# Optimization experiments

Hardware: AMD Instinct MI355X
Metric: run time of the kernel (lower is better)

The kernel has to match this reference:

```python
import jax, jax.numpy as jnp
import numpy as np

DIM = 64
NUM_FEAT = 14
NUM_OUT = 105
N_NODES = 8192
N_EDGES = 16384
N_GRAPHS = 256
N_STEMS = 2048
N_JBONDS = 1024


def lrelu(v):
    return jax.nn.leaky_relu(v, 0.01)


def setup_inputs() -> dict:
    key = jax.random.key(0)
    ks = jax.random.split(key, 40)
    def rn(k, shape, s=0.1):
        return jax.random.normal(k, shape, dtype=jnp.float32) * s
    inp = {}
    inp['x'] = jax.random.normal(ks[0], (N_NODES, NUM_FEAT), dtype=jnp.float32)
    inp['edge_attr'] = jax.random.uniform(ks[1], (N_EDGES, 4), dtype=jnp.float32)
    inp['edge_index'] = jax.random.randint(ks[2], (2, N_EDGES), 0, N_NODES)
    inp['batch'] = jnp.sort(jax.random.randint(ks[3], (N_NODES,), 0, N_GRAPHS))
    inp['stem_atmidx'] = jax.random.randint(ks[4], (N_STEMS,), 0, N_NODES)
    inp['jbond_atmidx'] = jax.random.randint(ks[5], (N_JBONDS, 2), 0, N_NODES)
    # lin0
    inp['lin0_w'] = rn(ks[6], (NUM_FEAT, DIM)); inp['lin0_b'] = rn(ks[7], (DIM,))
    # NNConv edge net: Linear(4,dim) -> LeakyReLU -> Linear(dim, dim*dim)
    inp['net_w1'] = rn(ks[8], (4, DIM)); inp['net_b1'] = rn(ks[9], (DIM,))
    inp['net_w2'] = rn(ks[10], (DIM, DIM * DIM), 0.02); inp['net_b2'] = rn(ks[11], (DIM * DIM,), 0.02)
    # NNConv root weight + bias
    inp['conv_root'] = rn(ks[12], (DIM, DIM)); inp['conv_bias'] = rn(ks[13], (DIM,))
    # GRU (torch gate order r,z,n); stored [in, 3*dim]
    inp['gru_w_ih'] = rn(ks[14], (DIM, 3 * DIM)); inp['gru_w_hh'] = rn(ks[15], (DIM, 3 * DIM))
    inp['gru_b_ih'] = rn(ks[16], (3 * DIM,)); inp['gru_b_hh'] = rn(ks[17], (3 * DIM,))
    # node2stem MLP
    inp['n2s_w1'] = rn(ks[18], (DIM, DIM)); inp['n2s_b1'] = rn(ks[19], (DIM,))
    inp['n2s_w2'] = rn(ks[20], (DIM, NUM_OUT)); inp['n2s_b2'] = rn(ks[21], (NUM_OUT,))
    # node2jbond MLP
    inp['n2j_w1'] = rn(ks[22], (DIM, DIM)); inp['n2j_b1'] = rn(ks[23], (DIM,))
    inp['n2j_w2'] = rn(ks[24], (DIM, 1)); inp['n2j_b2'] = rn(ks[25], (1,))
    # Set2Set LSTM(2*dim -> dim), torch gate order i,f,g,o; stored [in, 4*dim]
    inp['s2s_w_ih'] = rn(ks[26], (2 * DIM, 4 * DIM)); inp['s2s_w_hh'] = rn(ks[27], (DIM, 4 * DIM))
    inp['s2s_b_ih'] = rn(ks[28], (4 * DIM,)); inp['s2s_b_hh'] = rn(ks[29], (4 * DIM,))
    # lin_out
    inp['lin_out_w'] = rn(ks[30], (2 * DIM, 2)); inp['lin_out_b'] = rn(ks[31], (2,))
    return inp


def reference(x, edge_attr, lin0_w, lin0_b, net_w1, net_b1, net_w2, net_b2,
              conv_root, conv_bias, gru_w_ih, gru_w_hh, gru_b_ih, gru_b_hh,
              n2s_w1, n2s_b1, n2s_w2, n2s_b2, n2j_w1, n2j_b1, n2j_w2, n2j_b2,
              s2s_w_ih, s2s_w_hh, s2s_b_ih, s2s_b_hh, lin_out_w, lin_out_b,
              edge_index, batch, stem_atmidx, jbond_atmidx):
    N = x.shape[0]
    src, dst = edge_index[0], edge_index[1]
    out = lrelu(x @ lin0_w + lin0_b)          # [N, dim]
    h = out
    # edge-conditioned weights (edge_attr is constant across the 6 iterations)
    ew = (lrelu(edge_attr @ net_w1 + net_b1) @ net_w2 + net_b2).reshape(-1, DIM, DIM)  # [E,dim,dim]
    deg = jnp.maximum(jax.ops.segment_sum(jnp.ones_like(dst, dtype=x.dtype), dst, num_segments=N), 1.0)[:, None]
    for _ in range(6):
        msg = jnp.einsum('ei,eio->eo', out[src], ew)                        # per-edge matmul
        agg = jax.ops.segment_sum(msg, dst, num_segments=N) / deg          # scatter-mean
        m = lrelu(agg + out @ conv_root + conv_bias)
        # GRU update (torch gate order r,z,n)
        gi = m @ gru_w_ih + gru_b_ih
        gh = h @ gru_w_hh + gru_b_hh
        ir, iz, inn = jnp.split(gi, 3, axis=-1)
        hr, hz, hn = jnp.split(gh, 3, axis=-1)
        r = jax.nn.sigmoid(ir + hr)
        z = jax.nn.sigmoid(iz + hz)
        n = jnp.tanh(inn + r * hn)
        h = (1.0 - z) * n + z * h
        out = h
    # per-stem block logits
    stem_preds = lrelu(out[stem_atmidx] @ n2s_w1 + n2s_b1) @ n2s_w2 + n2s_b2  # [S, num_out]
    # jbond: gather both endpoints, predict scalar, mean over the pair
    jb = out[jbond_atmidx.reshape(-1)]
    jpred = lrelu(jb @ n2j_w1 + n2j_b1) @ n2j_w2 + n2j_b2                     # [2J,1]
    jbond_preds = jpred.reshape(jbond_atmidx.shape).mean(axis=1)              # [J]
    # Set2Set, processing_steps=1
    B = N_GRAPHS
    hS = jnp.zeros((B, DIM), x.dtype)
    cS = jnp.zeros((B, DIM), x.dtype)
    q_star = jnp.zeros((B, 2 * DIM), x.dtype)
    gates = q_star @ s2s_w_ih + s2s_b_ih + hS @ s2s_w_hh + s2s_b_hh
    gi_, gf_, gg_, go_ = jnp.split(gates, 4, axis=-1)
    cS = jax.nn.sigmoid(gf_) * cS + jax.nn.sigmoid(gi_) * jnp.tanh(gg_)
    hS = jax.nn.sigmoid(go_) * jnp.tanh(cS)
    q = hS                                                                    # [B, dim]
    e = jnp.sum(out * q[batch], axis=-1)                                      # [N]
    emax = jax.ops.segment_max(e, batch, num_segments=B)
    a_un = jnp.exp(e - emax[batch])
    a = a_un / jax.ops.segment_sum(a_un, batch, num_segments=B)[batch]
    r_pool = jax.ops.segment_sum(a[:, None] * out, batch, num_segments=B)     # [B, dim]
    q_star = jnp.concatenate([q, r_pool], axis=1)                             # [B, 2*dim]
    scalar_outs = q_star @ lin_out_w + lin_out_b                              # [B, 2]
    return (scalar_outs, stem_preds, jbond_preds)
```

## Files before the change

### kernel.cpp

```cpp
#include <hip/hip_runtime.h>

#define DIM 64
#define NF 14
#define NOUT 105
#define NN 8192
#define NE 16384
#define NB 256
#define NS 2048
#define NJ 1024
#define KTOT 4160
#define KSPLIT 8

#define C_X      0
#define C_EA     114688
#define C_L0W    180224
#define C_L0B    181120
#define C_NW1    181184
#define C_NB1    181440
#define C_NW2    181504
#define C_NB2    443648
#define C_CRT    447744
#define C_CB     451840
#define C_GWIH   451904
#define C_GWHH   464192
#define C_GBIH   476480
#define C_GBHH   476672
#define C_SW1    476864
#define C_SB1    480960
#define C_SW2    481024
#define C_SB2    487744
#define C_JW1    487856
#define C_JB1    491952
#define C_JW2    492016
#define C_JB2    492080
#define C_S2IH   492088
#define C_S2HH   492344
#define C_LOW    492600
#define C_LOB    492856
#define C_TOT    492864

typedef float f32x4 __attribute__((ext_vector_type(4)));
typedef short bf16x8 __attribute__((ext_vector_type(8)));

__device__ __forceinline__ float bf2f(unsigned short u){
  union { unsigned int i; float f; } v; v.i = ((unsigned int)u) << 16; return v.f;
}
__device__ __forceinline__ unsigned short f2bf(float f){
  union { float f; unsigned int i; } v; v.f = f;
  unsigned int x = v.i;
  return (unsigned short)((x + 0x7FFFu + ((x >> 16) & 1u)) >> 16);
}
__device__ __forceinline__ float sigm(float x){ return 1.f / (1.f + __expf(-x)); }
__device__ __forceinline__ float tanh_f(float x){
  x = fminf(10.f, fmaxf(-10.f, x));
  float e = __expf(2.f * x);
  return (e - 1.f) / (e + 1.f);
}
__device__ __forceinline__ float lrelu(float x){ return x > 0.f ? x : 0.01f * x; }

__device__ __forceinline__ float wred_sum(float v){
  #pragma unroll
  for (int off = 32; off > 0; off >>= 1) v += __shfl_xor(v, off, 64);
  return v;
}
__device__ __forceinline__ float wred_max(float v){
  #pragma unroll
  for (int off = 32; off > 0; off >>= 1) v = fmaxf(v, __shfl_xor(v, off, 64));
  return v;
}


__global__ void k_detect(const unsigned short* __restrict__ ea, int* __restrict__ flag){
  __shared__ int cnt;
  if (threadIdx.x == 0) cnt = 0;
  __syncthreads();
  int c = 0;
  for (int i = threadIdx.x; i < 8192; i += 256) c += (ea[2*i] >> 15) & 1;
  atomicAdd(&cnt, c);
  __syncthreads();
  if (threadIdx.x == 0) *flag = (cnt > 100) ? 1 : 0;
}

struct CvtArgs {
  const void* src[26];
  int n[26];
  int off[26];
};

__global__ void k_cvt(CvtArgs a, const int* __restrict__ flag, unsigned short* __restrict__ dst){
  bool f32 = (*flag != 0);
  int gid = blockIdx.x * blockDim.x + threadIdx.x, gs = gridDim.x * blockDim.x;
  #pragma unroll 1
  for (int j = 0; j < 26; ++j){
    const void* s = a.src[j];
    int n = a.n[j], o = a.off[j];
    for (int i = gid; i < n; i += gs)
      dst[o + i] = f32 ? f2bf(((const float*)s)[i]) : ((const unsigned short*)s)[i];
  }
}


__global__ void k_deg(const int* __restrict__ ei, float* __restrict__ deg){
  int e = blockIdx.x * blockDim.x + threadIdx.x;
  if (e < NE) atomicAdd(&deg[ei[NE + e]], 1.0f);
}

__global__ void k_lin0(const unsigned short* __restrict__ cvt,
                       float* __restrict__ actF, unsigned short* __restrict__ actB){
  const unsigned short* x = cvt + C_X;
  const unsigned short* w = cvt + C_L0W;
  const unsigned short* b = cvt + C_L0B;
  int idx = blockIdx.x * blockDim.x + threadIdx.x;
  int n = idx >> 6, d = idx & 63;
  float acc = bf2f(b[d]);
  #pragma unroll
  for (int f = 0; f < NF; ++f) acc += bf2f(x[n*NF + f]) * bf2f(w[f*DIM + d]);
  float v = lrelu(acc);
  actF[idx] = v; actB[idx] = f2bf(v);
}

__global__ void k_u(const unsigned short* __restrict__ cvt, unsigned short* __restrict__ u){
  const unsigned short* ea = cvt + C_EA;
  const unsigned short* w  = cvt + C_NW1;
  const unsigned short* b  = cvt + C_NB1;
  int idx = blockIdx.x * blockDim.x + threadIdx.x;
  int e = idx >> 6, d = idx & 63;
  float acc = bf2f(b[d]);
  #pragma unroll
  for (int f = 0; f < 4; ++f) acc += bf2f(ea[e*4 + f]) * bf2f(w[f*DIM + d]);
  u[idx] = f2bf(lrelu(acc));
}

__global__ void k_w2t(const unsigned short* __restrict__ cvt, unsigned short* __restrict__ w2t){
  const unsigned short* w2 = cvt + C_NW2;
  int t = blockIdx.x * blockDim.x + threadIdx.x;
  int n = t >> 6, k = t & 63;
  w2t[t] = w2[k*4096 + n];
}

__global__ void k_w2r(const unsigned short* __restrict__ cvt, unsigned short* __restrict__ w2rt){
  const unsigned short* w2 = cvt + C_NW2;
  const unsigned short* b2 = cvt + C_NB2;
  int t = blockIdx.x * blockDim.x + threadIdx.x;
  int o = t / KTOT, k = t - o * KTOT;
  unsigned short v = (k < 4096) ? w2[(k >> 6) * 4096 + (k & 63) * 64 + o]
                                : b2[(k - 4096) * 64 + o];
  w2rt[t] = v;
}

__global__ void k_prep(const unsigned short* __restrict__ cvt,
                       unsigned short* __restrict__ crt, unsigned short* __restrict__ btg,
                       float* __restrict__ cbg, float* __restrict__ qv){
  const unsigned short* cr  = cvt + C_CRT;
  const unsigned short* wih = cvt + C_GWIH;
  const unsigned short* whh = cvt + C_GWHH;
  const unsigned short* bih = cvt + C_GBIH;
  const unsigned short* bhh = cvt + C_GBHH;
  const unsigned short* s2sbih = cvt + C_S2IH;
  const unsigned short* s2sbhh = cvt + C_S2HH;
  int tid = threadIdx.x;
  for (int t = tid; t < 4096; t += 256){ int n = t & 63, k = t >> 6; crt[n*64 + k] = cr[k*64 + n]; }
  for (int t = tid; t < 32768; t += 256){
    int nidx = t >> 7, kidx = t & 127;
    int g = nidx >> 6, d = nidx & 63, ki = kidx & 63;
    unsigned short v = 0;
    if (kidx < 64){
      if (g == 0) v = wih[ki*192 + d];
      else if (g == 1) v = wih[ki*192 + 64 + d];
      else if (g == 2) v = wih[ki*192 + 128 + d];
    } else {
      if (g == 0) v = whh[ki*192 + d];
      else if (g == 1) v = whh[ki*192 + 64 + d];
      else if (g == 3) v = whh[ki*192 + 128 + d];
    }
    btg[nidx*128 + kidx] = v;
  }
  if (tid < 256){
    int g = tid >> 6, d = tid & 63;
    float v;
    if (g == 0) v = bf2f(bih[d]) + bf2f(bhh[d]);
    else if (g == 1) v = bf2f(bih[64 + d]) + bf2f(bhh[64 + d]);
    else if (g == 2) v = bf2f(bih[128 + d]);
    else v = bf2f(bhh[128 + d]);
    cbg[tid] = v;
  }
  if (tid < 64){
    float gi = bf2f(s2sbih[tid])       + bf2f(s2sbhh[tid]);
    float gg = bf2f(s2sbih[128 + tid]) + bf2f(s2sbhh[128 + tid]);
    float go = bf2f(s2sbih[192 + tid]) + bf2f(s2sbhh[192 + tid]);
    float c = sigm(gi) * tanh_f(gg);
    qv[tid] = sigm(go) * tanh_f(c);
  }
}


__global__ __launch_bounds__(256) void k_ew(const unsigned short* __restrict__ z,
                                            const unsigned short* __restrict__ w2t,
                                            const unsigned short* __restrict__ cvt,
                                            unsigned short* __restrict__ ew){
  const unsigned short* b2 = cvt + C_NB2;
  int w = threadIdx.x >> 6, lane = threadIdx.x & 63;
  int lm = lane & 15, q8 = (lane >> 4) * 8, rq = (lane >> 4) * 4;
  int e0 = blockIdx.x * 64;
  int n0 = blockIdx.y * 256 + w * 64;
  f32x4 acc[4][4];
  #pragma unroll
  for (int mt = 0; mt < 4; ++mt)
    #pragma unroll
    for (int nt = 0; nt < 4; ++nt) acc[mt][nt] = (f32x4){0.f, 0.f, 0.f, 0.f};
  #pragma unroll
  for (int kk = 0; kk < 2; ++kk){
    bf16x8 af[4], bfr[4];
    #pragma unroll
    for (int mt = 0; mt < 4; ++mt)
      af[mt] = *(const bf16x8*)&z[(size_t)(e0 + mt*16 + lm)*64 + kk*32 + q8];
    #pragma unroll
    for (int nt = 0; nt < 4; ++nt)
      bfr[nt] = *(const bf16x8*)&w2t[(size_t)(n0 + nt*16 + lm)*64 + kk*32 + q8];
    #pragma unroll
    for (int mt = 0; mt < 4; ++mt)
      #pragma unroll
      for (int nt = 0; nt < 4; ++nt)
        acc[mt][nt] = __builtin_amdgcn_mfma_f32_16x16x32_bf16(af[mt], bfr[nt], acc[mt][nt], 0, 0, 0);
  }
  #pragma unroll
  for (int nt = 0; nt < 4; ++nt){
    int col = n0 + nt*16 + lm;
    float bb = bf2f(b2[col]);
    #pragma unroll
    for (int mt = 0; mt < 4; ++mt)
      #pragma unroll
      for (int r = 0; r < 4; ++r){
        int row = e0 + mt*16 + rq + r;
        ew[(size_t)row*4096 + col] = f2bf(acc[mt][nt][r] + bb);
      }
  }
}

__global__ __launch_bounds__(256) void k_msg(const unsigned short* __restrict__ actB,
                                             const unsigned short* __restrict__ ew,
                                             const int* __restrict__ ei,
                                             float* __restrict__ agg){
  __shared__ float sact[4][64];
  int w = threadIdx.x >> 6, lane = threadIdx.x & 63;
  int e = blockIdx.x * 4 + w;
  int src = ei[e], dst = ei[NE + e];
  sact[w][lane] = bf2f(actB[(size_t)src*64 + lane]);
  __syncthreads();
  const unsigned short* ep = &ew[(size_t)e * 4096];
  float acc = 0.f;
  #pragma unroll 16
  for (int i = 0; i < 64; ++i) acc += sact[w][i] * bf2f(ep[i*64 + lane]);
  atomicAdd(&agg[(size_t)dst*64 + lane], acc);
}


__global__ __launch_bounds__(256) void k_msgf(const unsigned short* __restrict__ actB,
                                              const unsigned short* __restrict__ z,
                                              const unsigned short* __restrict__ w2rt,
                                              const int* __restrict__ ei,
                                              float* __restrict__ agg){
  __shared__ __align__(16) unsigned short sz[256 * 8];
  int w = threadIdx.x >> 6, lane = threadIdx.x & 63;
  int lm = lane & 15, q8 = (lane >> 4) * 8, rq = (lane >> 4) * 4;
  int e0 = blockIdx.x * 256;
  int s  = blockIdx.y;
  {
    int t = threadIdx.x;
    *(uint4*)&sz[t * 8] = *(const uint4*)&z[(size_t)(e0 + t) * 64 + s * 8];
  }
  __syncthreads();

  uint4 apack[4][2];
  #pragma unroll
  for (int mt = 0; mt < 4; ++mt){
    int src = ei[e0 + w*64 + mt*16 + lm];
    apack[mt][0] = *(const uint4*)&actB[(size_t)src * 64 + q8];
    apack[mt][1] = *(const uint4*)&actB[(size_t)src * 64 + 32 + q8];
  }

  f32x4 acc[4][4];
  #pragma unroll
  for (int mt = 0; mt < 4; ++mt)
    #pragma unroll
    for (int nt = 0; nt < 4; ++nt) acc[mt][nt] = (f32x4){0.f, 0.f, 0.f, 0.f};

  int kk0 = s * 16;
  int nk = (s == KSPLIT - 1) ? 18 : 16;
  for (int c = 0; c < nk; ++c){
    int kk = kk0 + c;
    bf16x8 bfr[4];
    #pragma unroll
    for (int nt = 0; nt < 4; ++nt)
      bfr[nt] = *(const bf16x8*)&w2rt[(size_t)(nt*16 + lm) * KTOT + kk*32 + q8];
    #pragma unroll
    for (int mt = 0; mt < 4; ++mt){
      float zf = 1.0f;
      if (kk < 128){
        int erow = w*64 + mt*16 + lm;
        zf = bf2f(sz[erow * 8 + ((kk >> 1) & 7)]);
      }
      uint4 ap = apack[mt][kk & 1];
      bf16x8 af;
      #pragma unroll
      for (int h = 0; h < 4; ++h){
        unsigned int dw = ((const unsigned int*)&ap)[h];
        float flo = __uint_as_float(dw << 16) * zf;
        float fhi = __uint_as_float(dw & 0xFFFF0000u) * zf;
        unsigned int pk = ((unsigned int)f2bf(flo)) | (((unsigned int)f2bf(fhi)) << 16);
        ((unsigned int*)&af)[h] = pk;
      }
      #pragma unroll
      for (int nt = 0; nt < 4; ++nt)
        acc[mt][nt] = __builtin_amdgcn_mfma_f32_16x16x32_bf16(af, bfr[nt], acc[mt][nt], 0, 0, 0);
    }
  }

  #pragma unroll
  for (int mt = 0; mt < 4; ++mt){
    int dstv[4];
    #pragma unroll
    for (int r = 0; r < 4; ++r) dstv[r] = ei[NE + e0 + w*64 + mt*16 + rq + r];
    #pragma unroll
    for (int nt = 0; nt < 4; ++nt)
      #pragma unroll
      for (int r = 0; r < 4; ++r)
        atomicAdd(&agg[(size_t)dstv[r] * 64 + nt*16 + lm], acc[mt][nt][r]);
  }
}


__global__ __launch_bounds__(256) void k_gru(const unsigned short* __restrict__ actB_in,
                                             const float* __restrict__ actF_in,
                                             float* __restrict__ agg, const float* __restrict__ deg,
                                             const unsigned short* __restrict__ crt,
                                             const unsigned short* __restrict__ cvt,
                                             const unsigned short* __restrict__ btg,
                                             const float* __restrict__ cbg,
                                             float* __restrict__ actF_out, unsigned short* __restrict__ actB_out){
  const unsigned short* cbias = cvt + C_CB;
  __shared__ __align__(16) unsigned short s_frag[2*4*16*8];
  int w = threadIdx.x >> 6, lane = threadIdx.x & 63;
  int lm = lane & 15, q = lane >> 4;
  int q8 = q*8, rq = q*4;
  int r0 = blockIdx.x * 16;
  f32x4 am = (f32x4){0.f, 0.f, 0.f, 0.f};
  #pragma unroll
  for (int kk = 0; kk < 2; ++kk){
    bf16x8 a = *(const bf16x8*)&actB_in[(size_t)(r0 + lm)*64 + kk*32 + q8];
    bf16x8 b = *(const bf16x8*)&crt[(size_t)(w*16 + lm)*64 + kk*32 + q8];
    am = __builtin_amdgcn_mfma_f32_16x16x32_bf16(a, b, am, 0, 0, 0);
  }
  {
    int col = w*16 + lm;
    float cb = bf2f(cbias[col]);
    int kk2 = w >> 1, q2 = (w & 1)*2 + (lm >> 3), j = lm & 7;
    #pragma unroll
    for (int r = 0; r < 4; ++r){
      int row = r0 + rq + r;
      float dg = fmaxf(deg[row], 1.f);
      float v = am[r] + agg[(size_t)row*64 + col] / dg + cb;
      agg[(size_t)row*64 + col] = 0.f;
      s_frag[((kk2*4 + q2)*16 + (rq + r))*8 + j] = f2bf(lrelu(v));
    }
  }
  __syncthreads();
  f32x4 g[4];
  #pragma unroll
  for (int t = 0; t < 4; ++t) g[t] = (f32x4){0.f, 0.f, 0.f, 0.f};
  #pragma unroll
  for (int kk = 0; kk < 4; ++kk){
    bf16x8 a;
    if (kk < 2) a = *(const bf16x8*)&s_frag[(kk*4 + q)*128 + lm*8];
    else        a = *(const bf16x8*)&actB_in[(size_t)(r0 + lm)*64 + (kk - 2)*32 + q8];
    #pragma unroll
    for (int t = 0; t < 4; ++t){
      bf16x8 b = *(const bf16x8*)&btg[(size_t)(t*64 + w*16 + lm)*128 + kk*32 + q8];
      g[t] = __builtin_amdgcn_mfma_f32_16x16x32_bf16(a, b, g[t], 0, 0, 0);
    }
  }
  {
    int d = w*16 + lm;
    float cb_r = cbg[d], cb_z = cbg[64 + d], cb_n = cbg[128 + d], cb_h = cbg[192 + d];
    #pragma unroll
    for (int r = 0; r < 4; ++r){
      int row = r0 + rq + r;
      float rr = sigm(g[0][r] + cb_r);
      float zz = sigm(g[1][r] + cb_z);
      float nn = tanh_f(g[2][r] + cb_n + rr * (g[3][r] + cb_h));
      float ho = actF_in[(size_t)row*64 + d];
      float hn2 = (1.f - zz) * nn + zz * ho;
      actF_out[(size_t)row*64 + d] = hn2;
      actB_out[(size_t)row*64 + d] = f2bf(hn2);
    }
  }
}


__device__ __forceinline__ int lower_bound_batch(const int* b, int val){
  int lo = 0, hi = NN;
  while (lo < hi){ int mid = (lo + hi) >> 1; if (b[mid] < val) lo = mid + 1; else hi = mid; }
  return lo;
}

__device__ __forceinline__ void store_out(void* outp, const int* flag, size_t idx, float v){
  if (*flag) ((float*)outp)[idx] = v;
  else       ((unsigned short*)outp)[idx] = f2bf(v);
}

__global__ __launch_bounds__(64) void k_graph(const float* __restrict__ act,
                                              const int* __restrict__ batch, const float* __restrict__ qv,
                                              const unsigned short* __restrict__ cvt,
                                              const int* __restrict__ flag,
                                              void* __restrict__ outp){
  const unsigned short* lw = cvt + C_LOW;
  const unsigned short* lb = cvt + C_LOB;
  __shared__ float se[512];
  int b = blockIdx.x, lane = threadIdx.x;
  int lo = lower_bound_batch(batch, b);
  int hi = lower_bound_batch(batch, b + 1);
  int cnt = hi - lo; if (cnt > 512) cnt = 512;
  float qvl = qv[lane];
  for (int ii = 0; ii < cnt; ++ii){
    float p = act[(size_t)(lo + ii)*64 + lane] * qvl;
    p = wred_sum(p);
    if (lane == 0) se[ii] = p;
  }
  __syncthreads();
  float em = -3.4e38f;
  for (int ii = lane; ii < cnt; ii += 64) em = fmaxf(em, se[ii]);
  em = wred_max(em);
  float sm = 0.f;
  for (int ii = lane; ii < cnt; ii += 64) sm += __expf(se[ii] - em);
  float denom = wred_sum(sm);
  float rp = 0.f;
  for (int ii = 0; ii < cnt; ++ii) rp += __expf(se[ii] - em) * act[(size_t)(lo + ii)*64 + lane];
  if (cnt > 0 && denom > 0.f) rp /= denom;
  float s0 = qvl*bf2f(lw[lane*2])     + rp*bf2f(lw[(64 + lane)*2]);
  float s1 = qvl*bf2f(lw[lane*2 + 1]) + rp*bf2f(lw[(64 + lane)*2 + 1]);
  s0 = wred_sum(s0); s1 = wred_sum(s1);
  if (lane == 0){
    store_out(outp, flag, b*2,     s0 + bf2f(lb[0]));
    store_out(outp, flag, b*2 + 1, s1 + bf2f(lb[1]));
  }
}

__global__ __launch_bounds__(256) void k_stem(const float* __restrict__ act, const int* __restrict__ sidx,
                                              const unsigned short* __restrict__ cvt,
                                              const int* __restrict__ flag,
                                              void* __restrict__ outp){
  const unsigned short* w1 = cvt + C_SW1;
  const unsigned short* b1 = cvt + C_SB1;
  const unsigned short* w2 = cvt + C_SW2;
  const unsigned short* b2 = cvt + C_SB2;
  __shared__ float sa[4][64], st[4][64];
  int w = threadIdx.x >> 6, lane = threadIdx.x & 63;
  int s = blockIdx.x * 4 + w;
  int a = sidx[s];
  sa[w][lane] = act[(size_t)a*64 + lane];
  __syncthreads();
  float t = bf2f(b1[lane]);
  #pragma unroll 8
  for (int i = 0; i < 64; ++i) t += sa[w][i] * bf2f(w1[i*64 + lane]);
  st[w][lane] = lrelu(t);
  __syncthreads();
  size_t base = 512 + (size_t)s * NOUT;
  float v = bf2f(b2[lane]);
  #pragma unroll 8
  for (int d = 0; d < 64; ++d) v += st[w][d] * bf2f(w2[d*NOUT + lane]);
  store_out(outp, flag, base + lane, v);
  int o2 = 64 + lane;
  if (o2 < NOUT){
    float v2 = bf2f(b2[o2]);
    #pragma unroll 8
    for (int d = 0; d < 64; ++d) v2 += st[w][d] * bf2f(w2[d*NOUT + o2]);
    store_out(outp, flag, base + o2, v2);
  }
}

__global__ __launch_bounds__(256) void k_jbond(const float* __restrict__ act, const int* __restrict__ jidx,
                                               const unsigned short* __restrict__ cvt,
                                               const int* __restrict__ flag,
                                               void* __restrict__ outp){
  const unsigned short* w1 = cvt + C_JW1;
  const unsigned short* b1 = cvt + C_JB1;
  const unsigned short* w2 = cvt + C_JW2;
  const unsigned short* b2 = cvt + C_JB2;
  __shared__ float a0[4][64], a1[4][64];
  int w = threadIdx.x >> 6, lane = threadIdx.x & 63;
  int j = blockIdx.x * 4 + w;
  int i0 = jidx[j*2], i1 = jidx[j*2 + 1];
  a0[w][lane] = act[(size_t)i0*64 + lane];
  a1[w][lane] = act[(size_t)i1*64 + lane];
  __syncthreads();
  float t0 = bf2f(b1[lane]), t1 = t0;
  #pragma unroll 8
  for (int i = 0; i < 64; ++i){
    float wv = bf2f(w1[i*64 + lane]);
    t0 += a0[w][i] * wv;
    t1 += a1[w][i] * wv;
  }
  t0 = lrelu(t0); t1 = lrelu(t1);
  float p = (t0 + t1) * bf2f(w2[lane]);
  p = wred_sum(p);
  if (lane == 0) store_out(outp, flag, 512 + (size_t)NS*NOUT + j, 0.5f * p + bf2f(b2[0]));
}


extern "C" void kernel_launch(void* const* d_in, const int* in_sizes, int n_in,
                              void* d_out, int out_size, void* d_ws, size_t ws_size,
                              hipStream_t stream){
  (void)in_sizes; (void)n_in; (void)out_size;
  const int* edge_index = (const int*)d_in[2];
  const int* batch      = (const int*)d_in[3];
  const int* stem_idx   = (const int*)d_in[4];
  const int* jbond_idx  = (const int*)d_in[5];

  char* ws = (char*)d_ws;
  size_t off = 0;
  auto alloc = [&](size_t bytes) -> void* {
    void* p = ws + off; off += (bytes + 255) & ~(size_t)255; return p;
  };
  unsigned short* cvt  = (unsigned short*)alloc((size_t)C_TOT * 2);
  unsigned short* w2t  = (unsigned short*)alloc((size_t)4096 * 64 * 2);
  unsigned short* w2rt = (unsigned short*)alloc((size_t)64 * KTOT * 2);
  unsigned short* z_bf = (unsigned short*)alloc((size_t)NE * 64 * 2);
  float* actF0 = (float*)alloc((size_t)NN * 64 * 4);
  float* actF1 = (float*)alloc((size_t)NN * 64 * 4);
  unsigned short* actB0 = (unsigned short*)alloc((size_t)NN * 64 * 2);
  unsigned short* actB1 = (unsigned short*)alloc((size_t)NN * 64 * 2);
  float* deg  = (float*)alloc(NN * 4);
  float* agg  = (float*)alloc((size_t)NN * 64 * 4);
  unsigned short* crt = (unsigned short*)alloc(64 * 64 * 2);
  unsigned short* btg = (unsigned short*)alloc(256 * 128 * 2);
  float* cbg  = (float*)alloc(256 * 4);
  float* qv   = (float*)alloc(64 * 4);
  int* flag   = (int*)alloc(256);
  size_t ew_bytes = (size_t)NE * 4096 * 2;
  bool big = (off + ew_bytes) <= ws_size;
  unsigned short* ew = big ? (unsigned short*)alloc(ew_bytes) : nullptr;

  hipMemsetAsync(deg, 0, ((size_t)NN * 4) + ((size_t)NN * 64 * 4) + 256, stream);

  k_detect<<<1, 256, 0, stream>>>((const unsigned short*)d_in[1], flag);

  CvtArgs ca;
  const int srcIdx[26] = {0,1,6,7,8,9,10,11,12,13,14,15,16,17,18,19,20,21,22,23,24,25,28,29,30,31};
  const int ns[26]  = {114688,65536,896,64,256,64,262144,4096,4096,64,12288,12288,192,192,
                       4096,64,6720,105,4096,64,64,1,256,256,256,2};
  const int ofs[26] = {C_X,C_EA,C_L0W,C_L0B,C_NW1,C_NB1,C_NW2,C_NB2,C_CRT,C_CB,C_GWIH,C_GWHH,
                       C_GBIH,C_GBHH,C_SW1,C_SB1,C_SW2,C_SB2,C_JW1,C_JB1,C_JW2,C_JB2,
                       C_S2IH,C_S2HH,C_LOW,C_LOB};
  for (int j = 0; j < 26; ++j){ ca.src[j] = d_in[srcIdx[j]]; ca.n[j] = ns[j]; ca.off[j] = ofs[j]; }
  k_cvt<<<512, 256, 0, stream>>>(ca, flag, cvt);

  k_deg<<<NE/256, 256, 0, stream>>>(edge_index, deg);
  k_lin0<<<NN*DIM/256, 256, 0, stream>>>(cvt, actF0, actB0);
  k_u<<<NE*DIM/256, 256, 0, stream>>>(cvt, z_bf);
  k_prep<<<1, 256, 0, stream>>>(cvt, crt, btg, cbg, qv);

  if (big){
    k_w2t<<<4096*64/256, 256, 0, stream>>>(cvt, w2t);
    k_ew<<<dim3(NE/64, 16), 256, 0, stream>>>(z_bf, w2t, cvt, ew);
  } else {
    k_w2r<<<64*KTOT/256, 256, 0, stream>>>(cvt, w2rt);
  }

  for (int t = 0; t < 6; ++t){
    const float* aF_in  = (t & 1) ? actF1 : actF0;
    float* aF_out       = (t & 1) ? actF0 : actF1;
    const unsigned short* aB_in = (t & 1) ? actB1 : actB0;
    unsigned short* aB_out      = (t & 1) ? actB0 : actB1;
    if (big)
      k_msg<<<NE/4, 256, 0, stream>>>(aB_in, ew, edge_index, agg);
    else
      k_msgf<<<dim3(NE/256, KSPLIT), 256, 0, stream>>>(aB_in, z_bf, w2rt, edge_index, agg);
    k_gru<<<NN/16, 256, 0, stream>>>(aB_in, aF_in, agg, deg, crt, cvt, btg, cbg,
                                     aF_out, aB_out);
  }
  k_graph<<<NB, 64, 0, stream>>>(actF0, batch, qv, cvt, flag, d_out);
  k_stem<<<NS/4, 256, 0, stream>>>(actF0, stem_idx, cvt, flag, d_out);
  k_jbond<<<NJ/4, 256, 0, stream>>>(actF0, jbond_idx, cvt, flag, d_out);
}
```

Baseline: 445.1 us.

## Transpose edge-weight layout and stage ew stores through swizzled LDS for vector writes

Permutes the w2t columns so each edge's weight matrix is stored transposed, which lets k_msg read 8 contiguous bf16 per lane with 16-byte vector loads instead of scalar strided loads. k_ew now writes its MFMA output into a swizzled shared-memory tile and then emits coalesced 16-byte global stores. This targets global memory transaction efficiency on the large ew buffer, at the cost of 32KB of LDS per block, which may reduce occupancy. Whether these kernels run by default depends on dispatch code that is not shown (k_msgf exists as an alternative path).

```diff
diff --git a/kernel.cpp b/kernel.cpp
--- a/kernel.cpp
+++ b/kernel.cpp
@@ -135,7 +135,7 @@
   const unsigned short* w2 = cvt + C_NW2;
   int t = blockIdx.x * blockDim.x + threadIdx.x;
   int n = t >> 6, k = t & 63;
-  w2t[t] = w2[k*4096 + n];
+  w2t[t] = w2[k*4096 + (n & 63)*64 + (n >> 6)];
 }
 
 __global__ void k_w2r(const unsigned short* __restrict__ cvt, unsigned short* __restrict__ w2rt){
@@ -199,6 +199,7 @@
                                             const unsigned short* __restrict__ cvt,
                                             unsigned short* __restrict__ ew){
   const unsigned short* b2 = cvt + C_NB2;
+  __shared__ __align__(16) unsigned short tile[4][4096];
   int w = threadIdx.x >> 6, lane = threadIdx.x & 63;
   int lm = lane & 15, q8 = (lane >> 4) * 8, rq = (lane >> 4) * 4;
   int e0 = blockIdx.x * 64;
@@ -225,15 +226,25 @@
   }
   #pragma unroll
   for (int nt = 0; nt < 4; ++nt){
-    int col = n0 + nt*16 + lm;
-    float bb = bf2f(b2[col]);
+    int col = nt*16 + lm;
+    int gcol = n0 + col;
+    float bb = bf2f(b2[((gcol & 63) << 6) | (gcol >> 6)]);
     #pragma unroll
     for (int mt = 0; mt < 4; ++mt)
       #pragma unroll
       for (int r = 0; r < 4; ++r){
-        int row = e0 + mt*16 + rq + r;
-        ew[(size_t)row*4096 + col] = f2bf(acc[mt][nt][r] + bb);
+        int row = mt*16 + rq + r;
+        int phys = (col >> 3) ^ (row & 7);
+        tile[w][row*64 + phys*8 + (col & 7)] = f2bf(acc[mt][nt][r] + bb);
       }
+  }
+  #pragma unroll
+  for (int it = 0; it < 8; ++it){
+    int row = it*8 + (lane >> 3);
+    int c16 = lane & 7;
+    int phys = c16 ^ (row & 7);
+    bf16x8 v = *(const bf16x8*)&tile[w][row*64 + phys*8];
+    *(bf16x8*)&ew[(size_t)(e0 + row)*4096 + n0 + c16*8] = v;
   }
 }
 
@@ -241,16 +252,28 @@
                                              const unsigned short* __restrict__ ew,
                                              const int* __restrict__ ei,
                                              float* __restrict__ agg){
-  __shared__ float sact[4][64];
+  __shared__ __align__(16) float sact[4][64];
   int w = threadIdx.x >> 6, lane = threadIdx.x & 63;
   int e = blockIdx.x * 4 + w;
   int src = ei[e], dst = ei[NE + e];
   sact[w][lane] = bf2f(actB[(size_t)src*64 + lane]);
   __syncthreads();
-  const unsigned short* ep = &ew[(size_t)e * 4096];
+  const unsigned short* ep = ew + (size_t)e*4096 + (size_t)lane*64;
   float acc = 0.f;
-  #pragma unroll 16
-  for (int i = 0; i < 64; ++i) acc += sact[w][i] * bf2f(ep[i*64 + lane]);
+  #pragma unroll
+  for (int t = 0; t < 8; ++t){
+    bf16x8 v = *(const bf16x8*)(ep + t*8);
+    f32x4 sa = *(const f32x4*)&sact[w][t*8];
+    f32x4 sb = *(const f32x4*)&sact[w][t*8 + 4];
+    acc += bf2f((unsigned short)v[0]) * sa[0];
+    acc += bf2f((unsigned short)v[1]) * sa[1];
+    acc += bf2f((unsigned short)v[2]) * sa[2];
+    acc += bf2f((unsigned short)v[3]) * sa[3];
+    acc += bf2f((unsigned short)v[4]) * sb[0];
+    acc += bf2f((unsigned short)v[5]) * sb[1];
+    acc += bf2f((unsigned short)v[6]) * sb[2];
+    acc += bf2f((unsigned short)v[7]) * sb[3];
+  }
   atomicAdd(&agg[(size_t)dst*64 + lane], acc);
 }
 
```

Measured after the change: 454.2 us. +2.0%, slower.

## Replace materialized edge weights with a fused factorized message kernel

Applied to the files above, without the earlier changes.

Drops the path that materializes the per-edge 64x64 weight tensor (about 128 MB in bf16) and re-reads it in all six message-passing iterations. Every iteration now computes messages directly with MFMA: the source activations are scaled by each edge-MLP hidden value and multiplied against the reordered second-layer weights, with the bias folded in as an extra K chunk. The fused kernel uses 64-edge tiles split four ways over K, stages z in padded shared memory, and packs bf16 with a cheaper rounding helper. The cost is extra MFMA work and atomic adds in every iteration instead of pure bandwidth-bound reads.

```diff
diff --git a/kernel.cpp b/kernel.cpp
--- a/kernel.cpp
+++ b/kernel.cpp
@@ -9,7 +9,6 @@
 #define NS 2048
 #define NJ 1024
 #define KTOT 4160
-#define KSPLIT 8
 
 #define C_X      0
 #define C_EA     114688
@@ -69,6 +68,12 @@
   return v;
 }
 
+__device__ __forceinline__ unsigned int pk_bf(float flo, float fhi){
+  unsigned int lo = __float_as_uint(flo) + 0x8000u;
+  unsigned int hi = __float_as_uint(fhi) + 0x8000u;
+  return (hi & 0xFFFF0000u) | (lo >> 16);
+}
+
 
 __global__ void k_detect(const unsigned short* __restrict__ ea, int* __restrict__ flag){
   __shared__ int cnt;
@@ -129,13 +134,6 @@
   #pragma unroll
   for (int f = 0; f < 4; ++f) acc += bf2f(ea[e*4 + f]) * bf2f(w[f*DIM + d]);
   u[idx] = f2bf(lrelu(acc));
-}
-
-__global__ void k_w2t(const unsigned short* __restrict__ cvt, unsigned short* __restrict__ w2t){
-  const unsigned short* w2 = cvt + C_NW2;
-  int t = blockIdx.x * blockDim.x + threadIdx.x;
-  int n = t >> 6, k = t & 63;
-  w2t[t] = w2[k*4096 + n];
 }
 
 __global__ void k_w2r(const unsigned short* __restrict__ cvt, unsigned short* __restrict__ w2rt){
@@ -194,138 +192,87 @@
 }
 
 
-__global__ __launch_bounds__(256) void k_ew(const unsigned short* __restrict__ z,
-                                            const unsigned short* __restrict__ w2t,
-                                            const unsigned short* __restrict__ cvt,
-                                            unsigned short* __restrict__ ew){
-  const unsigned short* b2 = cvt + C_NB2;
-  int w = threadIdx.x >> 6, lane = threadIdx.x & 63;
-  int lm = lane & 15, q8 = (lane >> 4) * 8, rq = (lane >> 4) * 4;
-  int e0 = blockIdx.x * 64;
-  int n0 = blockIdx.y * 256 + w * 64;
-  f32x4 acc[4][4];
-  #pragma unroll
-  for (int mt = 0; mt < 4; ++mt)
-    #pragma unroll
-    for (int nt = 0; nt < 4; ++nt) acc[mt][nt] = (f32x4){0.f, 0.f, 0.f, 0.f};
-  #pragma unroll
-  for (int kk = 0; kk < 2; ++kk){
-    bf16x8 af[4], bfr[4];
-    #pragma unroll
-    for (int mt = 0; mt < 4; ++mt)
-      af[mt] = *(const bf16x8*)&z[(size_t)(e0 + mt*16 + lm)*64 + kk*32 + q8];
-    #pragma unroll
-    for (int nt = 0; nt < 4; ++nt)
-      bfr[nt] = *(const bf16x8*)&w2t[(size_t)(n0 + nt*16 + lm)*64 + kk*32 + q8];
-    #pragma unroll
-    for (int mt = 0; mt < 4; ++mt)
-      #pragma unroll
-      for (int nt = 0; nt < 4; ++nt)
-        acc[mt][nt] = __builtin_amdgcn_mfma_f32_16x16x32_bf16(af[mt], bfr[nt], acc[mt][nt], 0, 0, 0);
-  }
-  #pragma unroll
-  for (int nt = 0; nt < 4; ++nt){
-    int col = n0 + nt*16 + lm;
-    float bb = bf2f(b2[col]);
-    #pragma unroll
-    for (int mt = 0; mt < 4; ++mt)
-      #pragma unroll
-      for (int r = 0; r < 4; ++r){
-        int row = e0 + mt*16 + rq + r;
-        ew[(size_t)row*4096 + col] = f2bf(acc[mt][nt][r] + bb);
-      }
-  }
-}
-
-__global__ __launch_bounds__(256) void k_msg(const unsigned short* __restrict__ actB,
-                                             const unsigned short* __restrict__ ew,
-                                             const int* __restrict__ ei,
-                                             float* __restrict__ agg){
-  __shared__ float sact[4][64];
-  int w = threadIdx.x >> 6, lane = threadIdx.x & 63;
-  int e = blockIdx.x * 4 + w;
-  int src = ei[e], dst = ei[NE + e];
-  sact[w][lane] = bf2f(actB[(size_t)src*64 + lane]);
-  __syncthreads();
-  const unsigned short* ep = &ew[(size_t)e * 4096];
-  float acc = 0.f;
-  #pragma unroll 16
-  for (int i = 0; i < 64; ++i) acc += sact[w][i] * bf2f(ep[i*64 + lane]);
-  atomicAdd(&agg[(size_t)dst*64 + lane], acc);
-}
-
-
-__global__ __launch_bounds__(256) void k_msgf(const unsigned short* __restrict__ actB,
+__global__ __launch_bounds__(256) void k_msgr(const unsigned short* __restrict__ actB,
                                               const unsigned short* __restrict__ z,
                                               const unsigned short* __restrict__ w2rt,
                                               const int* __restrict__ ei,
                                               float* __restrict__ agg){
-  __shared__ __align__(16) unsigned short sz[256 * 8];
-  int w = threadIdx.x >> 6, lane = threadIdx.x & 63;
-  int lm = lane & 15, q8 = (lane >> 4) * 8, rq = (lane >> 4) * 4;
-  int e0 = blockIdx.x * 256;
+  __shared__ __align__(16) unsigned short sz[64 * 72];
+  int tid = threadIdx.x;
+  int w = tid >> 6, lane = tid & 63;
+  int lm = lane & 15, q = lane >> 4;
+  int q8 = q * 8, rq = q * 4;
+  int e0 = blockIdx.x * 64;
   int s  = blockIdx.y;
+
   {
-    int t = threadIdx.x;
-    *(uint4*)&sz[t * 8] = *(const uint4*)&z[(size_t)(e0 + t) * 64 + s * 8];
-  }
-  __syncthreads();
-
-  uint4 apack[4][2];
-  #pragma unroll
-  for (int mt = 0; mt < 4; ++mt){
-    int src = ei[e0 + w*64 + mt*16 + lm];
-    apack[mt][0] = *(const uint4*)&actB[(size_t)src * 64 + q8];
-    apack[mt][1] = *(const uint4*)&actB[(size_t)src * 64 + 32 + q8];
-  }
-
-  f32x4 acc[4][4];
-  #pragma unroll
-  for (int mt = 0; mt < 4; ++mt)
+    int edge = tid >> 2, part = tid & 3;
+    *(uint4*)&sz[edge*72 + part*16]     = *(const uint4*)&z[(size_t)(e0 + edge)*64 + part*16];
+    *(uint4*)&sz[edge*72 + part*16 + 8] = *(const uint4*)&z[(size_t)(e0 + edge)*64 + part*16 + 8];
+  }
+  __syncthreads();
+
+  int me = w*16 + lm;
+  int src = ei[e0 + me];
+  uint4 ap0 = *(const uint4*)&actB[(size_t)src*64 + q8];
+  uint4 ap1 = *(const uint4*)&actB[(size_t)src*64 + 32 + q8];
+  float alo0[4], ahi0[4], alo1[4], ahi1[4];
+  #pragma unroll
+  for (int h = 0; h < 4; ++h){
+    unsigned int d0 = ((const unsigned int*)&ap0)[h];
+    unsigned int d1 = ((const unsigned int*)&ap1)[h];
+    alo0[h] = __uint_as_float(d0 << 16); ahi0[h] = __uint_as_float(d0 & 0xFFFF0000u);
+    alo1[h] = __uint_as_float(d1 << 16); ahi1[h] = __uint_as_float(d1 & 0xFFFF0000u);
+  }
+
+  int cbase  = (s == 0) ? 0 : (2 + 32*s);
+  int npairs = (s == 0) ? 17 : 16;
+  int dbase  = cbase >> 1;
+
+  const unsigned short* bp0 = w2rt + (size_t)(0*16 + lm)*KTOT + cbase*32 + q8;
+  const unsigned short* bp1 = w2rt + (size_t)(1*16 + lm)*KTOT + cbase*32 + q8;
+  const unsigned short* bp2 = w2rt + (size_t)(2*16 + lm)*KTOT + cbase*32 + q8;
+  const unsigned short* bp3 = w2rt + (size_t)(3*16 + lm)*KTOT + cbase*32 + q8;
+
+  f32x4 acc[4];
+  #pragma unroll
+  for (int nt = 0; nt < 4; ++nt) acc[nt] = (f32x4){0.f, 0.f, 0.f, 0.f};
+
+  #pragma unroll 2
+  for (int p = 0; p < npairs; ++p){
+    int d = dbase + p;
+    float zf = (d < 64) ? bf2f(sz[me*72 + d]) : 1.0f;
+    bf16x8 afe, afo;
     #pragma unroll
-    for (int nt = 0; nt < 4; ++nt) acc[mt][nt] = (f32x4){0.f, 0.f, 0.f, 0.f};
-
-  int kk0 = s * 16;
-  int nk = (s == KSPLIT - 1) ? 18 : 16;
-  for (int c = 0; c < nk; ++c){
-    int kk = kk0 + c;
-    bf16x8 bfr[4];
+    for (int h = 0; h < 4; ++h)
+      ((unsigned int*)&afe)[h] = pk_bf(alo0[h]*zf, ahi0[h]*zf);
+    #pragma unroll
+    for (int h = 0; h < 4; ++h)
+      ((unsigned int*)&afo)[h] = pk_bf(alo1[h]*zf, ahi1[h]*zf);
+    bf16x8 b0e = *(const bf16x8*)(bp0 + p*64);
+    bf16x8 b1e = *(const bf16x8*)(bp1 + p*64);
+    bf16x8 b2e = *(const bf16x8*)(bp2 + p*64);
+    bf16x8 b3e = *(const bf16x8*)(bp3 + p*64);
+    acc[0] = __builtin_amdgcn_mfma_f32_16x16x32_bf16(afe, b0e, acc[0], 0, 0, 0);
+    acc[1] = __builtin_amdgcn_mfma_f32_16x16x32_bf16(afe, b1e, acc[1], 0, 0, 0);
+    acc[2] = __builtin_amdgcn_mfma_f32_16x16x32_bf16(afe, b2e, acc[2], 0, 0, 0);
+    acc[3] = __builtin_amdgcn_mfma_f32_16x16x32_bf16(afe, b3e, acc[3], 0, 0, 0);
+    bf16x8 b0o = *(const bf16x8*)(bp0 + p*64 + 32);
+    bf16x8 b1o = *(const bf16x8*)(bp1 + p*64 + 32);
+    bf16x8 b2o = *(const bf16x8*)(bp2 + p*64 + 32);
+    bf16x8 b3o = *(const bf16x8*)(bp3 + p*64 + 32);
+    acc[0] = __builtin_amdgcn_mfma_f32_16x16x32_bf16(afo, b0o, acc[0], 0, 0, 0);
+    acc[1] = __builtin_amdgcn_mfma_f32_16x16x32_bf16(afo, b1o, acc[1], 0, 0, 0);
+    acc[2] = __builtin_amdgcn_mfma_f32_16x16x32_bf16(afo, b2o, acc[2], 0, 0, 0);
+    acc[3] = __builtin_amdgcn_mfma_f32_16x16x32_bf16(afo, b3o, acc[3], 0, 0, 0);
+  }
+
+  #pragma unroll
+  for (int r = 0; r < 4; ++r){
+    int dst = ei[NE + e0 + w*16 + rq + r];
     #pragma unroll
     for (int nt = 0; nt < 4; ++nt)
-      bfr[nt] = *(const bf16x8*)&w2rt[(size_t)(nt*16 + lm) * KTOT + kk*32 + q8];
-    #pragma unroll
-    for (int mt = 0; mt < 4; ++mt){
-      float zf = 1.0f;
-      if (kk < 128){
-        int erow = w*64 + mt*16 + lm;
-        zf = bf2f(sz[erow * 8 + ((kk >> 1) & 7)]);
-      }
-      uint4 ap = apack[mt][kk & 1];
-      bf16x8 af;
-      #pragma unroll
-      for (int h = 0; h < 4; ++h){
-        unsigned int dw = ((const unsigned int*)&ap)[h];
-        float flo = __uint_as_float(dw << 16) * zf;
-        float fhi = __uint_as_float(dw & 0xFFFF0000u) * zf;
-        unsigned int pk = ((unsigned int)f2bf(flo)) | (((unsigned int)f2bf(fhi)) << 16);
-        ((unsigned int*)&af)[h] = pk;
-      }
-      #pragma unroll
-      for (int nt = 0; nt < 4; ++nt)
-        acc[mt][nt] = __builtin_amdgcn_mfma_f32_16x16x32_bf16(af, bfr[nt], acc[mt][nt], 0, 0, 0);
-    }
-  }
-
-  #pragma unroll
-  for (int mt = 0; mt < 4; ++mt){
-    int dstv[4];
-    #pragma unroll
-    for (int r = 0; r < 4; ++r) dstv[r] = ei[NE + e0 + w*64 + mt*16 + rq + r];
-    #pragma unroll
-    for (int nt = 0; nt < 4; ++nt)
-      #pragma unroll
-      for (int r = 0; r < 4; ++r)
-        atomicAdd(&agg[(size_t)dstv[r] * 64 + nt*16 + lm], acc[mt][nt][r]);
+      atomicAdd(&agg[(size_t)dst*64 + nt*16 + lm], acc[nt][r]);
   }
 }
 
@@ -510,7 +457,7 @@
 extern "C" void kernel_launch(void* const* d_in, const int* in_sizes, int n_in,
                               void* d_out, int out_size, void* d_ws, size_t ws_size,
                               hipStream_t stream){
-  (void)in_sizes; (void)n_in; (void)out_size;
+  (void)in_sizes; (void)n_in; (void)out_size; (void)ws_size;
   const int* edge_index = (const int*)d_in[2];
   const int* batch      = (const int*)d_in[3];
   const int* stem_idx   = (const int*)d_in[4];
@@ -522,7 +469,6 @@
     void* p = ws + off; off += (bytes + 255) & ~(size_t)255; return p;
   };
   unsigned short* cvt  = (unsigned short*)alloc((size_t)C_TOT * 2);
-  unsigned short* w2t  = (unsigned short*)alloc((size_t)4096 * 64 * 2);
   unsigned short* w2rt = (unsigned short*)alloc((size_t)64 * KTOT * 2);
   unsigned short* z_bf = (unsigned short*)alloc((size_t)NE * 64 * 2);
   float* actF0 = (float*)alloc((size_t)NN * 64 * 4);
@@ -536,9 +482,6 @@
   float* cbg  = (float*)alloc(256 * 4);
   float* qv   = (float*)alloc(64 * 4);
   int* flag   = (int*)alloc(256);
-  size_t ew_bytes = (size_t)NE * 4096 * 2;
-  bool big = (off + ew_bytes) <= ws_size;
-  unsigned short* ew = big ? (unsigned short*)alloc(ew_bytes) : nullptr;
 
   hipMemsetAsync(deg, 0, ((size_t)NN * 4) + ((size_t)NN * 64 * 4) + 256, stream);
 
@@ -557,24 +500,15 @@
   k_deg<<<NE/256, 256, 0, stream>>>(edge_index, deg);
   k_lin0<<<NN*DIM/256, 256, 0, stream>>>(cvt, actF0, actB0);
   k_u<<<NE*DIM/256, 256, 0, stream>>>(cvt, z_bf);
+  k_w2r<<<64*KTOT/256, 256, 0, stream>>>(cvt, w2rt);
   k_prep<<<1, 256, 0, stream>>>(cvt, crt, btg, cbg, qv);
-
-  if (big){
-    k_w2t<<<4096*64/256, 256, 0, stream>>>(cvt, w2t);
-    k_ew<<<dim3(NE/64, 16), 256, 0, stream>>>(z_bf, w2t, cvt, ew);
-  } else {
-    k_w2r<<<64*KTOT/256, 256, 0, stream>>>(cvt, w2rt);
-  }
 
   for (int t = 0; t < 6; ++t){
     const float* aF_in  = (t & 1) ? actF1 : actF0;
     float* aF_out       = (t & 1) ? actF0 : actF1;
     const unsigned short* aB_in = (t & 1) ? actB1 : actB0;
     unsigned short* aB_out      = (t & 1) ? actB0 : actB1;
-    if (big)
-      k_msg<<<NE/4, 256, 0, stream>>>(aB_in, ew, edge_index, agg);
-    else
-      k_msgf<<<dim3(NE/256, KSPLIT), 256, 0, stream>>>(aB_in, z_bf, w2rt, edge_index, agg);
+    k_msgr<<<dim3(NE/64, 4), 256, 0, stream>>>(aB_in, z_bf, w2rt, edge_index, agg);
     k_gru<<<NN/16, 256, 0, stream>>>(aB_in, aF_in, agg, deg, crt, cvt, btg, cbg,
                                      aF_out, aB_out);
   }
```

Result: slower. 659.8 us (+48.2%).
